# Optimization experiments

Measured on AMD Instinct MI355X. Metric: run time of the kernel, lower is better.

## Reference

```python
import jax, jax.numpy as jnp
import numpy as np

B, M, D = 4, 2048, 1024


def setup_inputs() -> dict:
    key = jax.random.key(0)
    k1, k2, k3, k4 = jax.random.split(key, 4)
    x = jax.random.normal(k1, (B, M, D), dtype=jnp.float32)
    scale = 0.02
    wq = jax.random.normal(k2, (D, D), dtype=jnp.float32) * scale
    wk = jax.random.normal(k3, (D, D), dtype=jnp.float32) * scale
    wv = jax.random.normal(k4, (D, D), dtype=jnp.float32) * scale
    return {"x": x, "wq": wq, "wk": wk, "wv": wv}


def _rope_tables(m, d):
    # Faithful to source: phi = 10000 ** (-2*(i-1)/d)  (note the (i-1), incl. i=0)
    i = jnp.arange(d // 2, dtype=jnp.float32)
    phi = jnp.power(10000.0, -2.0 * (i - 1.0) / d)  # [d/2]
    pos = jnp.arange(m, dtype=jnp.float32)
    ang = pos[:, None] * phi[None, :]  # [m, d/2]
    return jnp.cos(ang), jnp.sin(ang)


def _apply_rope(t, cos, sin):
    # Original does t[pos] @ R[pos] (row-vector times rotation matrix):
    #   out_even =  t_even*cos + t_odd*sin
    #   out_odd  = -t_even*sin + t_odd*cos
    te = t[..., 0::2]  # [b, m, d/2]
    to = t[..., 1::2]
    oe = te * cos + to * sin
    oo = -te * sin + to * cos
    return jnp.stack([oe, oo], axis=-1).reshape(t.shape)


def reference(x, wq, wk, wv):
    b, m, d = x.shape
    q = x @ wq.T
    k = x @ wk.T
    v = x @ wv.T
    cos, sin = _rope_tables(m, d)
    qr = _apply_rope(q, cos, sin)
    kr = _apply_rope(k, cos, sin)
    # causal SDPA (dropout disabled for deterministic reference)
    scores = jnp.einsum('bqd,bkd->bqk', qr, kr) / jnp.sqrt(jnp.float32(d))
    causal = jnp.tril(jnp.ones((m, m), dtype=bool))
    scores = jnp.where(causal[None, :, :], scores, jnp.finfo(scores.dtype).min)
    attn = jax.nn.softmax(scores, axis=-1)
    return jnp.einsum('bqk,bkd->bqd', attn, v)
```

## Files before the change

### kernel.cpp

```cpp
#include <hip/hip_runtime.h>
#include <hip/hip_bf16.h>
#include <math.h>


typedef __bf16 bf16x8 __attribute__((ext_vector_type(8)));
typedef float  f32x4  __attribute__((ext_vector_type(4)));

__device__ __forceinline__ ushort f2bf(float f) {
    __hip_bfloat16 h = __float2bfloat16(f);
    return *reinterpret_cast<ushort*>(&h);
}

__device__ __forceinline__ void async_load16(const ushort* g, ushort* l) {
    __builtin_amdgcn_global_load_lds(
        (const __attribute__((address_space(1))) void*)g,
        (__attribute__((address_space(3))) void*)l, 16, 0, 0);
}

__global__ __launch_bounds__(256) void cvt_all_kernel(
    const float* __restrict__ x,  const float* __restrict__ wq,
    const float* __restrict__ wk, const float* __restrict__ wv,
    ushort* __restrict__ xb, ushort* __restrict__ wqb,
    ushort* __restrict__ wkb, ushort* __restrict__ wvb,
    float2* __restrict__ cs)
{
    const int t = blockIdx.y;
    if (t == 4) {
        const int idx = blockIdx.x * 256 + threadIdx.x;
        if (idx < 2048 * 512) {
            const int pos = idx >> 9, i = idx & 511;
            const float phi = powf(10000.0f, -2.0f * ((float)i - 1.0f) / 1024.0f);
            float s, c;
            sincosf((float)pos * phi, &s, &c);
            cs[idx] = make_float2(c, s);
        }
        return;
    }
    const float* in  = (t == 0) ? x  : (t == 1) ? wq  : (t == 2) ? wk  : wv;
    ushort*      out = (t == 0) ? xb : (t == 1) ? wqb : (t == 2) ? wkb : wvb;
    const int n4 = (t == 0) ? 2097152 : 262144;
    int i = blockIdx.x * blockDim.x + threadIdx.x;
    if (i < n4) {
        float4 f = ((const float4*)in)[i];
        ushort4 o;
        o.x = f2bf(f.x); o.y = f2bf(f.y); o.z = f2bf(f.z); o.w = f2bf(f.w);
        ((ushort4*)out)[i] = o;
    }
}

__device__ __forceinline__ void gemm128_core(
    const ushort* __restrict__ A, const ushort* __restrict__ B,
    int lda, int ldb, int m0, int n0, int kIters,
    ushort* As, ushort* Bs, f32x4 acc[4][4])
{
    const int tid  = threadIdx.x;
    const int lane = tid & 63, wave = tid >> 6;
    const int wm = (wave >> 1) * 64, wn = (wave & 1) * 64;
    const int quad = lane >> 4, l16 = lane & 15;
    const int srow = lane >> 2, c = lane & 3;
    const int rr   = wave * 32 + srow;
    const int cc   = c ^ ((rr >> 1) & 3);
    const int scol = cc * 8;

    const ushort* ag0 = A + (size_t)(m0 + rr) * lda + scol;
    const ushort* bg0 = B + (size_t)(n0 + rr) * ldb + scol;
    const ushort* ag1 = ag0 + (size_t)16 * lda;
    const ushort* bg1 = bg0 + (size_t)16 * ldb;
    ushort* la0 = As + (wave * 32) * 32;
    ushort* la1 = la0 + 16 * 32;
    ushort* lb0 = Bs + (wave * 32) * 32;
    ushort* lb1 = lb0 + 16 * 32;

    for (int kt = 0; kt < kIters; ++kt) {
        const int k0 = kt * 32;
        async_load16(ag0 + k0, la0);
        async_load16(ag1 + k0, la1);
        async_load16(bg0 + k0, lb0);
        async_load16(bg1 + k0, lb1);
        __syncthreads();
        bf16x8 aF[4], bF[4];
#pragma unroll
        for (int i = 0; i < 4; ++i) {
            const int r = wm + i * 16 + l16;
            aF[i] = *(const bf16x8*)(As + r * 32 + ((quad ^ ((r >> 1) & 3)) * 8));
        }
#pragma unroll
        for (int j = 0; j < 4; ++j) {
            const int r = wn + j * 16 + l16;
            bF[j] = *(const bf16x8*)(Bs + r * 32 + ((quad ^ ((r >> 1) & 3)) * 8));
        }
#pragma unroll
        for (int i = 0; i < 4; ++i)
#pragma unroll
            for (int j = 0; j < 4; ++j)
                acc[i][j] = __builtin_amdgcn_mfma_f32_16x16x32_bf16(aF[i], bF[j], acc[i][j], 0, 0, 0);
        __syncthreads();
    }
}

#define ACC_INIT4(acc) \
    _Pragma("unroll") for (int i = 0; i < 4; ++i) \
    _Pragma("unroll") for (int j = 0; j < 4; ++j) \
    _Pragma("unroll") for (int r = 0; r < 4; ++r) acc[i][j][r] = 0.0f;

__global__ __launch_bounds__(256) void qkv_rope_kernel(
    const ushort* __restrict__ xb, const ushort* __restrict__ wq,
    const ushort* __restrict__ wk, const ushort* __restrict__ wv,
    const float2* __restrict__ cs,
    ushort* __restrict__ Qr, ushort* __restrict__ Kr, ushort* __restrict__ VT)
{
    __shared__ __attribute__((aligned(16))) ushort As[128 * 32];
    __shared__ __attribute__((aligned(16))) ushort Bs[128 * 32];
    const int m0 = blockIdx.x * 128;
    const int n0 = blockIdx.y * 128;
    const int z  = blockIdx.z;
    const ushort* W = (z == 0) ? wq : (z == 1) ? wk : wv;

    f32x4 acc[4][4];
    ACC_INIT4(acc)
    gemm128_core(xb, W, 1024, 1024, m0, n0, 32, As, Bs, acc);

    const int lane = threadIdx.x & 63, wave = threadIdx.x >> 6;
    const int wm = (wave >> 1) * 64, wn = (wave & 1) * 64;
    const int quad = lane >> 4, l16 = lane & 15;

    if (z < 2) {
        ushort* out = (z == 0) ? Qr : Kr;
#pragma unroll
        for (int j = 0; j < 4; ++j) {
            const int n = n0 + wn + j * 16 + l16;
            const int iidx = n >> 1;
            const bool odd = n & 1;
#pragma unroll
            for (int i = 0; i < 4; ++i) {
                const int mbase = m0 + wm + i * 16 + quad * 4;
                const int pos0  = mbase & 2047;
                const float2* csp = cs + (size_t)pos0 * 512 + iidx;
#pragma unroll
                for (int r = 0; r < 4; ++r) {
                    const float2 sc = csp[(size_t)r * 512];
                    float v = acc[i][j][r];
                    float p = __shfl_xor(v, 1);
                    float o = odd ? (v * sc.x - p * sc.y) : (v * sc.x + p * sc.y);
                    out[(size_t)(mbase + r) * 1024 + n] = f2bf(o);
                }
            }
        }
    } else {
#pragma unroll
        for (int i = 0; i < 4; ++i) {
            const int mbase = m0 + wm + i * 16 + quad * 4;
            const int b = mbase >> 11, pos0 = mbase & 2047;
#pragma unroll
            for (int j = 0; j < 4; ++j) {
                const int n = n0 + wn + j * 16 + l16;
                ushort4 o;
                o.x = f2bf(acc[i][j][0]); o.y = f2bf(acc[i][j][1]);
                o.z = f2bf(acc[i][j][2]); o.w = f2bf(acc[i][j][3]);
                *(ushort4*)(VT + ((size_t)b * 1024 + n) * 2048 + pos0) = o;
            }
        }
    }
}

__global__ __launch_bounds__(256) void scores_kernel(
    const ushort* __restrict__ Qr, const ushort* __restrict__ Kr,
    float* __restrict__ S)
{
    const int m0 = blockIdx.x * 128;
    const int n0 = blockIdx.y * 128;
    if (n0 > m0 + 127) return;
    const int b = blockIdx.z;
    __shared__ __attribute__((aligned(16))) ushort As[128 * 32];
    __shared__ __attribute__((aligned(16))) ushort Bs[128 * 32];
    const ushort* A = Qr + (size_t)b * 2048 * 1024;
    const ushort* B = Kr + (size_t)b * 2048 * 1024;
    float* Sb = S + (size_t)b * 2048 * 2048;

    f32x4 acc[4][4];
    ACC_INIT4(acc)
    gemm128_core(A, B, 1024, 1024, m0, n0, 32, As, Bs, acc);

    const int lane = threadIdx.x & 63, wave = threadIdx.x >> 6;
    const int wm = (wave >> 1) * 64, wn = (wave & 1) * 64;
    const int quad = lane >> 4, l16 = lane & 15;
#pragma unroll
    for (int i = 0; i < 4; ++i)
#pragma unroll
        for (int j = 0; j < 4; ++j) {
            const int n = n0 + wn + j * 16 + l16;
#pragma unroll
            for (int r = 0; r < 4; ++r) {
                const int m = m0 + wm + i * 16 + quad * 4 + r;
                Sb[(size_t)m * 2048 + n] = acc[i][j][r] * 0.03125f;
            }
        }
}

__global__ __launch_bounds__(256) void softmax_kernel(
    const float* __restrict__ S, ushort* __restrict__ P)
{
    __shared__ float red[256];
    const int row = blockIdx.x, tid = threadIdx.x, b = blockIdx.y;
    const float* s = S + ((size_t)b * 2048 + row) * 2048;
    ushort*      p = P + ((size_t)b * 2048 + row) * 2048;
    const int nvalid = row + 1;
    const int wlimit = (row & ~127) + 128;
    const int j0 = tid * 8;

    float v[8] = {0.0f, 0.0f, 0.0f, 0.0f, 0.0f, 0.0f, 0.0f, 0.0f};
    if (j0 < nvalid) {
        float4 f0 = *(const float4*)(s + j0);
        v[0]=f0.x; v[1]=f0.y; v[2]=f0.z; v[3]=f0.w;
    }
    if (j0 + 4 < nvalid) {
        float4 f1 = *(const float4*)(s + j0 + 4);
        v[4]=f1.x; v[5]=f1.y; v[6]=f1.z; v[7]=f1.w;
    }

    float mx = -3.402823466e38f;
#pragma unroll
    for (int u = 0; u < 8; ++u) if (j0 + u < nvalid) mx = fmaxf(mx, v[u]);
    red[tid] = mx; __syncthreads();
    for (int off = 128; off > 0; off >>= 1) {
        if (tid < off) red[tid] = fmaxf(red[tid], red[tid + off]);
        __syncthreads();
    }
    mx = red[0]; __syncthreads();

    float sum = 0.0f;
#pragma unroll
    for (int u = 0; u < 8; ++u) {
        v[u] = (j0 + u < nvalid) ? __expf(v[u] - mx) : 0.0f;
        sum += v[u];
    }
    red[tid] = sum; __syncthreads();
    for (int off = 128; off > 0; off >>= 1) {
        if (tid < off) red[tid] += red[tid + off];
        __syncthreads();
    }
    const float inv = 1.0f / red[0];

    if (j0 < wlimit) {
        ushort o[8];
#pragma unroll
        for (int u = 0; u < 8; ++u) o[u] = f2bf(v[u] * inv);
        *(int4*)(p + j0) = *(const int4*)o;
    }
}

__global__ __launch_bounds__(256) void pv_kernel(
    const ushort* __restrict__ P, const ushort* __restrict__ VT,
    float* __restrict__ out)
{
    __shared__ __attribute__((aligned(16))) ushort As[128 * 32];
    __shared__ __attribute__((aligned(16))) ushort Bs[128 * 32];
    const int m0 = blockIdx.x * 128;
    const int n0 = blockIdx.y * 128;
    const int b  = blockIdx.z;
    const ushort* A = P + (size_t)b * 2048 * 2048;
    const ushort* B = VT + (size_t)b * 1024 * 2048;
    const int kIters = (m0 + 128) / 32;

    f32x4 acc[4][4];
    ACC_INIT4(acc)
    gemm128_core(A, B, 2048, 2048, m0, n0, kIters, As, Bs, acc);

    const int lane = threadIdx.x & 63, wave = threadIdx.x >> 6;
    const int wm = (wave >> 1) * 64, wn = (wave & 1) * 64;
    const int quad = lane >> 4, l16 = lane & 15;
#pragma unroll
    for (int i = 0; i < 4; ++i)
#pragma unroll
        for (int j = 0; j < 4; ++j) {
            const int n = n0 + wn + j * 16 + l16;
#pragma unroll
            for (int r = 0; r < 4; ++r) {
                const int m = m0 + wm + i * 16 + quad * 4 + r;
                out[((size_t)b * 2048 + m) * 1024 + n] = acc[i][j][r];
            }
        }
}

extern "C" void kernel_launch(void* const* d_in, const int* in_sizes, int n_in,
                              void* d_out, int out_size, void* d_ws, size_t ws_size,
                              hipStream_t stream) {
    const float* x  = (const float*)d_in[0];
    const float* wq = (const float*)d_in[1];
    const float* wk = (const float*)d_in[2];
    const float* wv = (const float*)d_in[3];

    const size_t MiB = 1024 * 1024;
    char* ws = (char*)d_ws;
    ushort* xb  = (ushort*)(ws);
    ushort* wqb = (ushort*)(ws +  16 * MiB);
    ushort* wkb = (ushort*)(ws +  18 * MiB);
    ushort* wvb = (ushort*)(ws +  20 * MiB);
    ushort* Qr  = (ushort*)(ws +  22 * MiB);
    ushort* Kr  = (ushort*)(ws +  38 * MiB);
    ushort* VT  = (ushort*)(ws +  54 * MiB);
    float*  S   = (float* )(ws +  70 * MiB);
    ushort* P   = (ushort*)(ws + 134 * MiB);
    float2* cs  = (float2*)(ws + 166 * MiB);
    float*  out = (float*)d_out;

    cvt_all_kernel <<<dim3(8192, 5),   256, 0, stream>>>(x, wq, wk, wv, xb, wqb, wkb, wvb, cs);
    qkv_rope_kernel<<<dim3(64, 8, 3),  256, 0, stream>>>(xb, wqb, wkb, wvb, cs, Qr, Kr, VT);
    scores_kernel  <<<dim3(16, 16, 4), 256, 0, stream>>>(Qr, Kr, S);
    softmax_kernel <<<dim3(2048, 4),   256, 0, stream>>>(S, P);
    pv_kernel      <<<dim3(16, 8, 4),  256, 0, stream>>>(P, VT, out);
}
```

Baseline: 292.0 us.

## Double-buffer LDS tiles in shared GEMM core to overlap loads with MFMA

Gives the shared 128x128 GEMM core two LDS buffers per operand and issues the async global-to-LDS loads for the next k-tile before computing on the current one. The aim is to hide global load latency behind MFMA work, where before the loop loaded a tile and then synced and computed in strict sequence. The cost is twice the LDS per block, which may lower occupancy. It also relies on the single end-of-iteration barrier to make the prefetched loads visible, and no explicit vmcnt wait is added for the global_load_lds operations.

```diff
diff --git a/kernel.cpp b/kernel.cpp
--- a/kernel.cpp
+++ b/kernel.cpp
@@ -66,28 +66,36 @@
     const ushort* bg0 = B + (size_t)(n0 + rr) * ldb + scol;
     const ushort* ag1 = ag0 + (size_t)16 * lda;
     const ushort* bg1 = bg0 + (size_t)16 * ldb;
-    ushort* la0 = As + (wave * 32) * 32;
-    ushort* la1 = la0 + 16 * 32;
-    ushort* lb0 = Bs + (wave * 32) * 32;
-    ushort* lb1 = lb0 + 16 * 32;
-
+    const int lofs = (wave * 32) * 32;
+
+    async_load16(ag0, As + lofs);
+    async_load16(ag1, As + lofs + 16 * 32);
+    async_load16(bg0, Bs + lofs);
+    async_load16(bg1, Bs + lofs + 16 * 32);
+    __syncthreads();
+
+    int cur = 0;
     for (int kt = 0; kt < kIters; ++kt) {
-        const int k0 = kt * 32;
-        async_load16(ag0 + k0, la0);
-        async_load16(ag1 + k0, la1);
-        async_load16(bg0 + k0, lb0);
-        async_load16(bg1 + k0, lb1);
-        __syncthreads();
+        if (kt + 1 < kIters) {
+            const int k1 = (kt + 1) * 32;
+            const int nb = (cur ^ 1) * 4096;
+            async_load16(ag0 + k1, As + nb + lofs);
+            async_load16(ag1 + k1, As + nb + lofs + 16 * 32);
+            async_load16(bg0 + k1, Bs + nb + lofs);
+            async_load16(bg1 + k1, Bs + nb + lofs + 16 * 32);
+        }
+        const ushort* as = As + cur * 4096;
+        const ushort* bs = Bs + cur * 4096;
         bf16x8 aF[4], bF[4];
 #pragma unroll
         for (int i = 0; i < 4; ++i) {
             const int r = wm + i * 16 + l16;
-            aF[i] = *(const bf16x8*)(As + r * 32 + ((quad ^ ((r >> 1) & 3)) * 8));
+            aF[i] = *(const bf16x8*)(as + r * 32 + ((quad ^ ((r >> 1) & 3)) * 8));
         }
 #pragma unroll
         for (int j = 0; j < 4; ++j) {
             const int r = wn + j * 16 + l16;
-            bF[j] = *(const bf16x8*)(Bs + r * 32 + ((quad ^ ((r >> 1) & 3)) * 8));
+            bF[j] = *(const bf16x8*)(bs + r * 32 + ((quad ^ ((r >> 1) & 3)) * 8));
         }
 #pragma unroll
         for (int i = 0; i < 4; ++i)
@@ -95,6 +103,7 @@
             for (int j = 0; j < 4; ++j)
                 acc[i][j] = __builtin_amdgcn_mfma_f32_16x16x32_bf16(aF[i], bF[j], acc[i][j], 0, 0, 0);
         __syncthreads();
+        cur ^= 1;
     }
 }
 
@@ -109,8 +118,8 @@
     const float2* __restrict__ cs,
     ushort* __restrict__ Qr, ushort* __restrict__ Kr, ushort* __restrict__ VT)
 {
-    __shared__ __attribute__((aligned(16))) ushort As[128 * 32];
-    __shared__ __attribute__((aligned(16))) ushort Bs[128 * 32];
+    __shared__ __attribute__((aligned(16))) ushort As[2 * 128 * 32];
+    __shared__ __attribute__((aligned(16))) ushort Bs[2 * 128 * 32];
     const int m0 = blockIdx.x * 128;
     const int n0 = blockIdx.y * 128;
     const int z  = blockIdx.z;
@@ -171,8 +180,8 @@
     const int n0 = blockIdx.y * 128;
     if (n0 > m0 + 127) return;
     const int b = blockIdx.z;
-    __shared__ __attribute__((aligned(16))) ushort As[128 * 32];
-    __shared__ __attribute__((aligned(16))) ushort Bs[128 * 32];
+    __shared__ __attribute__((aligned(16))) ushort As[2 * 128 * 32];
+    __shared__ __attribute__((aligned(16))) ushort Bs[2 * 128 * 32];
     const ushort* A = Qr + (size_t)b * 2048 * 1024;
     const ushort* B = Kr + (size_t)b * 2048 * 1024;
     float* Sb = S + (size_t)b * 2048 * 2048;
@@ -253,8 +262,8 @@
     const ushort* __restrict__ P, const ushort* __restrict__ VT,
     float* __restrict__ out)
 {
-    __shared__ __attribute__((aligned(16))) ushort As[128 * 32];
-    __shared__ __attribute__((aligned(16))) ushort Bs[128 * 32];
+    __shared__ __attribute__((aligned(16))) ushort As[2 * 128 * 32];
+    __shared__ __attribute__((aligned(16))) ushort Bs[2 * 128 * 32];
     const int m0 = blockIdx.x * 128;
     const int n0 = blockIdx.y * 128;
     const int b  = blockIdx.z;
```

New measurement: 285.5 us. -2.2%, faster.
